# Optimization experiments

Measured on AMD Instinct MI355X. Metric: run time of the kernel, lower is better.

## Reference

```python
import jax, jax.numpy as jnp
import numpy as np

NUM_HEADS = 12
LN_EPS = 1e-5


def _layernorm(x, w, b):
    m = jnp.mean(x, axis=-1, keepdims=True)
    v = jnp.mean(jnp.square(x - m), axis=-1, keepdims=True)
    return (x - m) * jax.lax.rsqrt(v + LN_EPS) * w + b


def setup_inputs() -> dict:
    key = jax.random.key(0)
    ks = jax.random.split(key, 6)
    B, N, C, H = 8, 1024, 768, 3072
    s = 0.02
    return {
        "x": jax.random.normal(ks[0], (B, N, C), jnp.float32),
        "ln1_w": jnp.ones((C,), jnp.float32),
        "ln1_b": jnp.zeros((C,), jnp.float32),
        "qkv_w": jax.random.normal(ks[1], (3 * C, C), jnp.float32) * s,
        "qkv_b": jnp.zeros((3 * C,), jnp.float32),
        "proj_w": jax.random.normal(ks[2], (C, C), jnp.float32) * s,
        "proj_b": jnp.zeros((C,), jnp.float32),
        "ln2_w": jnp.ones((C,), jnp.float32),
        "ln2_b": jnp.zeros((C,), jnp.float32),
        "fc1_w": jax.random.normal(ks[3], (H, C), jnp.float32) * s,
        "fc1_b": jnp.zeros((H,), jnp.float32),
        "fc2_w": jax.random.normal(ks[4], (C, H), jnp.float32) * s,
        "fc2_b": jnp.zeros((C,), jnp.float32),
    }


def reference(x, ln1_w, ln1_b, qkv_w, qkv_b, proj_w, proj_b,
              ln2_w, ln2_b, fc1_w, fc1_b, fc2_w, fc2_b):
    B, N, C = x.shape
    H = NUM_HEADS
    d = C // H
    scale = d ** (-0.5)

    # --- attention on norm1(x) (size=None path, dropout rates are 0) ---
    h = _layernorm(x, ln1_w, ln1_b)
    qkv = h @ qkv_w.T + qkv_b                      # [B,N,3C]
    qkv = qkv.reshape(B, N, 3, H, d).transpose(2, 0, 3, 1, 4)  # [3,B,H,N,d]
    q, k, v = qkv[0], qkv[1], qkv[2]
    attn = jnp.einsum('bhqd,bhkd->bhqk', q, k) * scale
    attn = jax.nn.softmax(attn, axis=-1)
    o = jnp.einsum('bhqk,bhkd->bhqd', attn, v)     # [B,H,N,d]
    o = o.transpose(0, 2, 1, 3).reshape(B, N, C)
    x_attn = o @ proj_w.T + proj_b

    # --- residual + MLP ---
    x = x + x_attn
    h2 = _layernorm(x, ln2_w, ln2_b)
    h2 = jax.nn.gelu(h2 @ fc1_w.T + fc1_b, approximate=False)
    x = x + (h2 @ fc2_w.T + fc2_b)
    return x
```

## Files before the change

kernel.cpp:

```cpp
#include <hip/hip_runtime.h>
#include <cmath>

typedef __bf16 bf16;
typedef __bf16 bf16x8 __attribute__((ext_vector_type(8)));
typedef __bf16 bf16x4 __attribute__((ext_vector_type(4)));
typedef float floatx4 __attribute__((ext_vector_type(4)));

#define MFMA16(A, B, C) __builtin_amdgcn_mfma_f32_16x16x32_bf16((A), (B), (C), 0, 0, 0)

#define GLDS16(g, l)                                                   \
  __builtin_amdgcn_global_load_lds(                                    \
      (const __attribute__((address_space(1))) void*)(g),              \
      (__attribute__((address_space(3))) void*)(l), 16, 0, 0)

__global__ __launch_bounds__(256) void f2b4_kernel(
    const float* __restrict__ s0, bf16* __restrict__ d0, int n0,
    const float* __restrict__ s1, bf16* __restrict__ d1, int n1,
    const float* __restrict__ s2, bf16* __restrict__ d2, int n2,
    const float* __restrict__ s3, bf16* __restrict__ d3, int n3) {
  int i = blockIdx.x * 256 + threadIdx.x;
  const float* s;
  bf16* d;
  if (i < n0) { s = s0 + (size_t)i * 4; d = d0 + (size_t)i * 4; }
  else if ((i -= n0) < n1) { s = s1 + (size_t)i * 4; d = d1 + (size_t)i * 4; }
  else if ((i -= n1) < n2) { s = s2 + (size_t)i * 4; d = d2 + (size_t)i * 4; }
  else if ((i -= n2) < n3) { s = s3 + (size_t)i * 4; d = d3 + (size_t)i * 4; }
  else return;
  bf16x4 v;
  v[0] = (bf16)s[0]; v[1] = (bf16)s[1]; v[2] = (bf16)s[2]; v[3] = (bf16)s[3];
  *(bf16x4*)d = v;
}

__global__ __launch_bounds__(256) void ln_kernel(const float* __restrict__ x,
                                                 const float* __restrict__ g,
                                                 const float* __restrict__ be,
                                                 bf16* __restrict__ out) {
  int row = blockIdx.x;
  int t = threadIdx.x;
  const float* xr = x + (size_t)row * 768;
  float v0 = xr[t], v1 = xr[t + 256], v2 = xr[t + 512];
  float s = v0 + v1 + v2;
  float s2 = v0 * v0 + v1 * v1 + v2 * v2;
#pragma unroll
  for (int o = 1; o < 64; o <<= 1) {
    s += __shfl_xor(s, o, 64);
    s2 += __shfl_xor(s2, o, 64);
  }
  __shared__ float red[8];
  int w = t >> 6, lane = t & 63;
  if (lane == 0) { red[w] = s; red[4 + w] = s2; }
  __syncthreads();
  float ts = red[0] + red[1] + red[2] + red[3];
  float ts2 = red[4] + red[5] + red[6] + red[7];
  float mean = ts * (1.0f / 768.0f);
  float var = ts2 * (1.0f / 768.0f) - mean * mean;
  float rstd = rsqrtf(var + 1e-5f);
  bf16* orow = out + (size_t)row * 768;
  orow[t]       = (bf16)((v0 - mean) * rstd * g[t]       + be[t]);
  orow[t + 256] = (bf16)((v1 - mean) * rstd * g[t + 256] + be[t + 256]);
  orow[t + 512] = (bf16)((v2 - mean) * rstd * g[t + 512] + be[t + 512]);
}

__global__ __launch_bounds__(256) void reduce_ln_kernel(
    const bf16* __restrict__ pp, const float* __restrict__ bias,
    const float* __restrict__ x, const float* __restrict__ g,
    const float* __restrict__ be, float* __restrict__ x1,
    bf16* __restrict__ h2) {
  int row = blockIdx.x;
  int t = threadIdx.x;
  const bf16* p0 = pp + (size_t)row * 768;
  const bf16* p1 = pp + (size_t)(8192 + row) * 768;
  const float* xr = x + (size_t)row * 768;
  float v0 = (float)p0[t]       + (float)p1[t]       + bias[t]       + xr[t];
  float v1 = (float)p0[t + 256] + (float)p1[t + 256] + bias[t + 256] + xr[t + 256];
  float v2 = (float)p0[t + 512] + (float)p1[t + 512] + bias[t + 512] + xr[t + 512];
  float* x1r = x1 + (size_t)row * 768;
  x1r[t] = v0; x1r[t + 256] = v1; x1r[t + 512] = v2;
  float s = v0 + v1 + v2;
  float s2 = v0 * v0 + v1 * v1 + v2 * v2;
#pragma unroll
  for (int o = 1; o < 64; o <<= 1) {
    s += __shfl_xor(s, o, 64);
    s2 += __shfl_xor(s2, o, 64);
  }
  __shared__ float red[8];
  int w = t >> 6, lane = t & 63;
  if (lane == 0) { red[w] = s; red[4 + w] = s2; }
  __syncthreads();
  float ts = red[0] + red[1] + red[2] + red[3];
  float ts2 = red[4] + red[5] + red[6] + red[7];
  float mean = ts * (1.0f / 768.0f);
  float var = ts2 * (1.0f / 768.0f) - mean * mean;
  float rstd = rsqrtf(var + 1e-5f);
  bf16* orow = h2 + (size_t)row * 768;
  orow[t]       = (bf16)((v0 - mean) * rstd * g[t]       + be[t]);
  orow[t + 256] = (bf16)((v1 - mean) * rstd * g[t + 256] + be[t + 256]);
  orow[t + 512] = (bf16)((v2 - mean) * rstd * g[t + 512] + be[t + 512]);
}

__global__ __launch_bounds__(256) void reduce_out_kernel(
    const bf16* __restrict__ pp, const float* __restrict__ bias,
    const float* __restrict__ x1, float* __restrict__ out) {
  int i = blockIdx.x * 256 + threadIdx.x;
  size_t base = (size_t)i * 4;
  int col = (int)(base % 768);
  bf16x4 a = *(const bf16x4*)(pp + base);
  bf16x4 b = *(const bf16x4*)(pp + (size_t)8192 * 768 + base);
  float4 xr = *(const float4*)(x1 + base);
  float4 r;
  r.x = (float)a[0] + (float)b[0] + bias[col]     + xr.x;
  r.y = (float)a[1] + (float)b[1] + bias[col + 1] + xr.y;
  r.z = (float)a[2] + (float)b[2] + bias[col + 2] + xr.z;
  r.w = (float)a[3] + (float)b[3] + bias[col + 3] + xr.w;
  *(float4*)(out + base) = r;
}

constexpr int EP_BF16 = 0;
constexpr int EP_PART = 1;
constexpr int EP_GELU_BF16 = 2;

template <int EP>
__global__ __launch_bounds__(256, 3) void gemm_bt(
    const bf16* __restrict__ A, const bf16* __restrict__ Bw,
    const float* __restrict__ bias,
    void* __restrict__ outp, int M, int N, int K) {
  __shared__ alignas(16) bf16 Asl[128 * 32];
  __shared__ alignas(16) bf16 Bsl[128 * 32];
  int tid = threadIdx.x;
  int lane = tid & 63, w = tid >> 6;
  int wm = w >> 1, wn = w & 1;
  int q16 = lane & 15, quad = lane >> 4;
  int fid = blockIdx.x + gridDim.x * blockIdx.y;
  int nb = gridDim.x;
  int s = fid >> 3;
  int m0 = ((fid & 7) * (gridDim.y >> 3) + s / nb) * 128;
  int n0 = (s % nb) * 128;
  int kz = blockIdx.z;
  int Ksub = K / gridDim.z;
  int kbeg = kz * Ksub;

  floatx4 acc[4][4];
#pragma unroll
  for (int i = 0; i < 4; i++)
#pragma unroll
    for (int j = 0; j < 4; j++) acc[i][j] = (floatx4){0.f, 0.f, 0.f, 0.f};

  int rA = (lane >> 2), c8 = (lane & 3) * 8;
  const bf16* a0 = A + (size_t)(m0 + (w * 2 + 0) * 16 + rA) * K + kbeg + c8;
  const bf16* a1 = A + (size_t)(m0 + (w * 2 + 1) * 16 + rA) * K + kbeg + c8;
  const bf16* b0 = Bw + (size_t)(n0 + (w * 2 + 0) * 16 + rA) * K + kbeg + c8;
  const bf16* b1 = Bw + (size_t)(n0 + (w * 2 + 1) * 16 + rA) * K + kbeg + c8;
  bf16* la0 = &Asl[w * 1024];
  bf16* la1 = &Asl[w * 1024 + 512];
  bf16* lb0 = &Bsl[w * 1024];
  bf16* lb1 = &Bsl[w * 1024 + 512];

  for (int k0 = 0; k0 < Ksub; k0 += 32) {
    __syncthreads();
    GLDS16(a0, la0);
    GLDS16(a1, la1);
    GLDS16(b0, lb0);
    GLDS16(b1, lb1);
    a0 += 32; a1 += 32; b0 += 32; b1 += 32;
    __syncthreads();
    bf16x8 af[4], bfr[4];
#pragma unroll
    for (int i = 0; i < 4; i++)
      af[i] = *(const bf16x8*)&Asl[(wm * 64 + i * 16 + q16) * 32 + quad * 8];
#pragma unroll
    for (int j = 0; j < 4; j++)
      bfr[j] = *(const bf16x8*)&Bsl[(wn * 64 + j * 16 + q16) * 32 + quad * 8];
#pragma unroll
    for (int i = 0; i < 4; i++)
#pragma unroll
      for (int j = 0; j < 4; j++) acc[i][j] = MFMA16(af[i], bfr[j], acc[i][j]);
  }

  bf16* opart = (bf16*)outp + (size_t)kz * M * N;
#pragma unroll
  for (int i = 0; i < 4; i++) {
#pragma unroll
    for (int j = 0; j < 4; j++) {
#pragma unroll
      for (int r = 0; r < 4; r++) {
        int m = m0 + wm * 64 + i * 16 + quad * 4 + r;
        int n = n0 + wn * 64 + j * 16 + q16;
        size_t idx = (size_t)m * N + n;
        if constexpr (EP == EP_PART) {
          opart[idx] = (bf16)acc[i][j][r];
        } else {
          float v = acc[i][j][r] + bias[n];
          if constexpr (EP == EP_BF16) {
            ((bf16*)outp)[idx] = (bf16)v;
          } else {
            float gv = 0.5f * v * (1.0f + erff(v * 0.70710678118654752f));
            ((bf16*)outp)[idx] = (bf16)gv;
          }
        }
      }
    }
  }
}

__global__ __launch_bounds__(256, 3) void attn_kernel(const bf16* __restrict__ qkv,
                                                      bf16* __restrict__ o) {
  __shared__ alignas(16) bf16 Kl[32 * 64];
  __shared__ alignas(16) bf16 Vt[64 * 5 * 8];
  __shared__ alignas(16) bf16 Pl[4][2][16 * 40];
  int tid = threadIdx.x;
  int lane = tid & 63, w = tid >> 6;
  int q16 = lane & 15, quad = lane >> 4;
  int b = blockIdx.y / 12, h = blockIdx.y % 12;
  int qbase = blockIdx.x * 128 + w * 32;

  bf16x8 qf[2][2];
#pragma unroll
  for (int qt = 0; qt < 2; qt++)
#pragma unroll
    for (int c = 0; c < 2; c++)
      qf[qt][c] = *(const bf16x8*)(qkv +
          (size_t)(b * 1024 + qbase + qt * 16 + q16) * 2304 + h * 64 +
          c * 32 + quad * 8);

  int kkey = w * 8 + (lane >> 3);
  int kchunk = (lane & 7) ^ (lane >> 3);
  const bf16* kg = qkv + (size_t)(b * 1024 + kkey) * 2304 + 768 + h * 64 +
                   (kchunk & 7) * 8;
  bf16* kl_dst = &Kl[w * 512];

  int kr = tid >> 3;
  int kcb = (tid & 7) * 8;
  const bf16* vg = qkv + (size_t)(b * 1024 + kr) * 2304 + 1536 + h * 64 + kcb;
  int vt_idx[8];
#pragma unroll
  for (int e = 0; e < 8; e++)
    vt_idx[e] = ((((kcb + e) * 5) + w) ^ (tid & 7)) * 8 + (kr & 7);

  int koff[2][2];
#pragma unroll
  for (int nc = 0; nc < 2; nc++)
#pragma unroll
    for (int ck = 0; ck < 2; ck++) {
      int key = nc * 16 + q16;
      koff[nc][ck] = (key * 8 + ((ck * 4 + quad) ^ (key & 7))) * 8;
    }
  int voff[4];
#pragma unroll
  for (int dc = 0; dc < 4; dc++) {
    int d = dc * 16 + q16;
    voff[dc] = ((d * 5 + quad) ^ ((d >> 3) & 7)) * 8;
  }
  const bf16* pread = &Pl[w][0][q16 * 40 + quad * 8];
  int pw_base = (quad * 4) * 40 + q16;

  float l_[2][4];
  floatx4 oacc[2][4];
#pragma unroll
  for (int qt = 0; qt < 2; qt++)
#pragma unroll
    for (int r = 0; r < 4; r++) l_[qt][r] = 0.f;
#pragma unroll
  for (int qt = 0; qt < 2; qt++)
#pragma unroll
    for (int dc = 0; dc < 4; dc++) oacc[qt][dc] = (floatx4){0.f, 0.f, 0.f, 0.f};

  for (int kt = 0; kt < 32; kt++) {
    __syncthreads();
    GLDS16(kg, kl_dst);
    bf16x8 vv = *(const bf16x8*)vg;
    kg += 32 * 2304;
    vg += 32 * 2304;
#pragma unroll
    for (int e = 0; e < 8; e++) Vt[vt_idx[e]] = vv[e];
    __syncthreads();

    bf16x8 kf[2][2];
#pragma unroll
    for (int nc = 0; nc < 2; nc++)
#pragma unroll
      for (int ck = 0; ck < 2; ck++)
        kf[nc][ck] = *(const bf16x8*)&Kl[koff[nc][ck]];

#pragma unroll
    for (int qt = 0; qt < 2; qt++) {
#pragma unroll
      for (int nc = 0; nc < 2; nc++) {
        floatx4 z = (floatx4){0.f, 0.f, 0.f, 0.f};
        z = MFMA16(qf[qt][0], kf[nc][0], z);
        z = MFMA16(qf[qt][1], kf[nc][1], z);
#pragma unroll
        for (int r = 0; r < 4; r++) {
          float p = __builtin_amdgcn_exp2f(z[r] * 0.18033688011f);
          l_[qt][r] += p;
          Pl[w][qt][pw_base + r * 40 + nc * 16] = (bf16)p;
        }
      }
    }
    __syncthreads();

    bf16x8 vf[4];
#pragma unroll
    for (int dc = 0; dc < 4; dc++) vf[dc] = *(const bf16x8*)&Vt[voff[dc]];
#pragma unroll
    for (int qt = 0; qt < 2; qt++) {
      bf16x8 pf = *(const bf16x8*)(pread + qt * 640);
#pragma unroll
      for (int dc = 0; dc < 4; dc++)
        oacc[qt][dc] = MFMA16(pf, vf[dc], oacc[qt][dc]);
    }
  }

#pragma unroll
  for (int qt = 0; qt < 2; qt++) {
    bf16* op = o + (size_t)(b * 1024 + qbase + qt * 16) * 768 + h * 64;
#pragma unroll
    for (int r = 0; r < 4; r++) {
      float s = l_[qt][r];
#pragma unroll
      for (int off = 1; off < 16; off <<= 1) s += __shfl_xor(s, off, 16);
      float inv = 1.0f / s;
#pragma unroll
      for (int dc = 0; dc < 4; dc++)
        op[(size_t)(quad * 4 + r) * 768 + dc * 16 + q16] =
            (bf16)(oacc[qt][dc][r] * inv);
    }
  }
}

extern "C" void kernel_launch(void* const* d_in, const int* in_sizes, int n_in,
                              void* d_out, int out_size, void* d_ws, size_t ws_size,
                              hipStream_t stream) {
  (void)in_sizes; (void)n_in; (void)out_size; (void)ws_size;
  const float* x      = (const float*)d_in[0];
  const float* ln1_w  = (const float*)d_in[1];
  const float* ln1_b  = (const float*)d_in[2];
  const float* qkv_w  = (const float*)d_in[3];
  const float* qkv_b  = (const float*)d_in[4];
  const float* proj_w = (const float*)d_in[5];
  const float* proj_b = (const float*)d_in[6];
  const float* ln2_w  = (const float*)d_in[7];
  const float* ln2_b  = (const float*)d_in[8];
  const float* fc1_w  = (const float*)d_in[9];
  const float* fc1_b  = (const float*)d_in[10];
  const float* fc2_w  = (const float*)d_in[11];
  const float* fc2_b  = (const float*)d_in[12];

  char* ws = (char*)d_ws;
  size_t off = 0;
  auto alloc = [&](size_t bytes) {
    void* p = ws + off;
    off += (bytes + 255) & ~(size_t)255;
    return p;
  };
  bf16* wq  = (bf16*)alloc((size_t)2304 * 768 * 2);
  bf16* wp  = (bf16*)alloc((size_t)768 * 768 * 2);
  bf16* wf1 = (bf16*)alloc((size_t)3072 * 768 * 2);
  bf16* wf2 = (bf16*)alloc((size_t)768 * 3072 * 2);
  bf16* slotA = (bf16*)alloc((size_t)8192 * 768 * 2);
  bf16* slotB = (bf16*)alloc((size_t)8192 * 3072 * 2);
  float* x1 = (float*)alloc((size_t)8192 * 768 * 4);
  bf16* part = (bf16*)alloc((size_t)2 * 8192 * 768 * 2);

  bf16* h1 = slotA;
  bf16* qkvb = slotB;
  bf16* ob = slotA;
  bf16* h2 = slotA;
  bf16* hm = slotB;

  f2b4_kernel<<<6912, 256, 0, stream>>>(
      qkv_w, wq, 2304 * 768 / 4, proj_w, wp, 768 * 768 / 4,
      fc1_w, wf1, 3072 * 768 / 4, fc2_w, wf2, 768 * 3072 / 4);

  ln_kernel<<<8192, 256, 0, stream>>>(x, ln1_w, ln1_b, h1);
  gemm_bt<EP_BF16><<<dim3(18, 64, 1), 256, 0, stream>>>(h1, wq, qkv_b, qkvb,
                                                        8192, 2304, 768);
  attn_kernel<<<dim3(8, 96), 256, 0, stream>>>(qkvb, ob);
  gemm_bt<EP_PART><<<dim3(6, 64, 2), 256, 0, stream>>>(ob, wp, nullptr, part,
                                                       8192, 768, 768);
  reduce_ln_kernel<<<8192, 256, 0, stream>>>(part, proj_b, x, ln2_w, ln2_b,
                                             x1, h2);
  gemm_bt<EP_GELU_BF16><<<dim3(24, 64, 1), 256, 0, stream>>>(h2, wf1, fc1_b, hm,
                                                             8192, 3072, 768);
  gemm_bt<EP_PART><<<dim3(6, 64, 2), 256, 0, stream>>>(hm, wf2, nullptr, part,
                                                       8192, 768, 3072);
  reduce_out_kernel<<<6144, 256, 0, stream>>>(part, fc2_b, x1, (float*)d_out);
}
```

Baseline: 372.6 us.

## Deepen GEMM K-tile to 64 with XOR swizzle, fuse LN1 with weight cast, approximate GELU

```diff
diff --git a/kernel.cpp b/kernel.cpp
--- a/kernel.cpp
+++ b/kernel.cpp
@@ -13,12 +13,41 @@
       (const __attribute__((address_space(1))) void*)(g),              \
       (__attribute__((address_space(3))) void*)(l), 16, 0, 0)
 
-__global__ __launch_bounds__(256) void f2b4_kernel(
+__global__ __launch_bounds__(256) void pre_kernel(
+    const float* __restrict__ x, const float* __restrict__ g,
+    const float* __restrict__ be, bf16* __restrict__ h1,
     const float* __restrict__ s0, bf16* __restrict__ d0, int n0,
     const float* __restrict__ s1, bf16* __restrict__ d1, int n1,
     const float* __restrict__ s2, bf16* __restrict__ d2, int n2,
     const float* __restrict__ s3, bf16* __restrict__ d3, int n3) {
-  int i = blockIdx.x * 256 + threadIdx.x;
+  int bid = blockIdx.x;
+  int t = threadIdx.x;
+  if (bid < 8192) {
+    const float* xr = x + (size_t)bid * 768;
+    float v0 = xr[t], v1 = xr[t + 256], v2 = xr[t + 512];
+    float s = v0 + v1 + v2;
+    float s2 = v0 * v0 + v1 * v1 + v2 * v2;
+#pragma unroll
+    for (int o = 1; o < 64; o <<= 1) {
+      s += __shfl_xor(s, o, 64);
+      s2 += __shfl_xor(s2, o, 64);
+    }
+    __shared__ float red[8];
+    int w = t >> 6, lane = t & 63;
+    if (lane == 0) { red[w] = s; red[4 + w] = s2; }
+    __syncthreads();
+    float ts = red[0] + red[1] + red[2] + red[3];
+    float ts2 = red[4] + red[5] + red[6] + red[7];
+    float mean = ts * (1.0f / 768.0f);
+    float var = ts2 * (1.0f / 768.0f) - mean * mean;
+    float rstd = rsqrtf(var + 1e-5f);
+    bf16* orow = h1 + (size_t)bid * 768;
+    orow[t]       = (bf16)((v0 - mean) * rstd * g[t]       + be[t]);
+    orow[t + 256] = (bf16)((v1 - mean) * rstd * g[t + 256] + be[t + 256]);
+    orow[t + 512] = (bf16)((v2 - mean) * rstd * g[t + 512] + be[t + 512]);
+    return;
+  }
+  int i = (bid - 8192) * 256 + t;
   const float* s;
   bf16* d;
   if (i < n0) { s = s0 + (size_t)i * 4; d = d0 + (size_t)i * 4; }
@@ -29,36 +58,6 @@
   bf16x4 v;
   v[0] = (bf16)s[0]; v[1] = (bf16)s[1]; v[2] = (bf16)s[2]; v[3] = (bf16)s[3];
   *(bf16x4*)d = v;
-}
-
-__global__ __launch_bounds__(256) void ln_kernel(const float* __restrict__ x,
-                                                 const float* __restrict__ g,
-                                                 const float* __restrict__ be,
-                                                 bf16* __restrict__ out) {
-  int row = blockIdx.x;
-  int t = threadIdx.x;
-  const float* xr = x + (size_t)row * 768;
-  float v0 = xr[t], v1 = xr[t + 256], v2 = xr[t + 512];
-  float s = v0 + v1 + v2;
-  float s2 = v0 * v0 + v1 * v1 + v2 * v2;
-#pragma unroll
-  for (int o = 1; o < 64; o <<= 1) {
-    s += __shfl_xor(s, o, 64);
-    s2 += __shfl_xor(s2, o, 64);
-  }
-  __shared__ float red[8];
-  int w = t >> 6, lane = t & 63;
-  if (lane == 0) { red[w] = s; red[4 + w] = s2; }
-  __syncthreads();
-  float ts = red[0] + red[1] + red[2] + red[3];
-  float ts2 = red[4] + red[5] + red[6] + red[7];
-  float mean = ts * (1.0f / 768.0f);
-  float var = ts2 * (1.0f / 768.0f) - mean * mean;
-  float rstd = rsqrtf(var + 1e-5f);
-  bf16* orow = out + (size_t)row * 768;
-  orow[t]       = (bf16)((v0 - mean) * rstd * g[t]       + be[t]);
-  orow[t + 256] = (bf16)((v1 - mean) * rstd * g[t + 256] + be[t + 256]);
-  orow[t + 512] = (bf16)((v2 - mean) * rstd * g[t + 512] + be[t + 512]);
 }
 
 __global__ __launch_bounds__(256) void reduce_ln_kernel(
@@ -124,8 +123,8 @@
     const bf16* __restrict__ A, const bf16* __restrict__ Bw,
     const float* __restrict__ bias,
     void* __restrict__ outp, int M, int N, int K) {
-  __shared__ alignas(16) bf16 Asl[128 * 32];
-  __shared__ alignas(16) bf16 Bsl[128 * 32];
+  __shared__ alignas(16) bf16 Asl[128 * 64];
+  __shared__ alignas(16) bf16 Bsl[128 * 64];
   int tid = threadIdx.x;
   int lane = tid & 63, w = tid >> 6;
   int wm = w >> 1, wn = w & 1;
@@ -145,35 +144,52 @@
 #pragma unroll
     for (int j = 0; j < 4; j++) acc[i][j] = (floatx4){0.f, 0.f, 0.f, 0.f};
 
-  int rA = (lane >> 2), c8 = (lane & 3) * 8;
-  const bf16* a0 = A + (size_t)(m0 + (w * 2 + 0) * 16 + rA) * K + kbeg + c8;
-  const bf16* a1 = A + (size_t)(m0 + (w * 2 + 1) * 16 + rA) * K + kbeg + c8;
-  const bf16* b0 = Bw + (size_t)(n0 + (w * 2 + 0) * 16 + rA) * K + kbeg + c8;
-  const bf16* b1 = Bw + (size_t)(n0 + (w * 2 + 1) * 16 + rA) * K + kbeg + c8;
-  bf16* la0 = &Asl[w * 1024];
-  bf16* la1 = &Asl[w * 1024 + 512];
-  bf16* lb0 = &Bsl[w * 1024];
-  bf16* lb1 = &Bsl[w * 1024 + 512];
-
-  for (int k0 = 0; k0 < Ksub; k0 += 32) {
-    __syncthreads();
-    GLDS16(a0, la0);
-    GLDS16(a1, la1);
-    GLDS16(b0, lb0);
-    GLDS16(b1, lb1);
-    a0 += 32; a1 += 32; b0 += 32; b1 += 32;
-    __syncthreads();
-    bf16x8 af[4], bfr[4];
-#pragma unroll
-    for (int i = 0; i < 4; i++)
-      af[i] = *(const bf16x8*)&Asl[(wm * 64 + i * 16 + q16) * 32 + quad * 8];
-#pragma unroll
-    for (int j = 0; j < 4; j++)
-      bfr[j] = *(const bf16x8*)&Bsl[(wn * 64 + j * 16 + q16) * 32 + quad * 8];
-#pragma unroll
-    for (int i = 0; i < 4; i++)
-#pragma unroll
-      for (int j = 0; j < 4; j++) acc[i][j] = MFMA16(af[i], bfr[j], acc[i][j]);
+  int rIn = lane >> 3;
+  int cg = (lane & 7) ^ rIn;
+  const bf16* ag[4];
+  const bf16* bg[4];
+#pragma unroll
+  for (int q = 0; q < 4; q++) {
+    int ca = w * 4 + q;
+    ag[q] = A + (size_t)(m0 + ca * 8 + rIn) * K + kbeg + cg * 8;
+    bg[q] = Bw + (size_t)(n0 + ca * 8 + rIn) * K + kbeg + cg * 8;
+  }
+  bf16* la = &Asl[w * 2048];
+  bf16* lb = &Bsl[w * 2048];
+
+  int msel = q16 & 7;
+  int offA[2][4], offB[2][4];
+#pragma unroll
+  for (int ks = 0; ks < 2; ks++) {
+#pragma unroll
+    for (int i = 0; i < 4; i++) {
+      offA[ks][i] = (wm * 64 + i * 16 + q16) * 64 + (((ks * 4 + quad) ^ msel)) * 8;
+      offB[ks][i] = (wn * 64 + i * 16 + q16) * 64 + (((ks * 4 + quad) ^ msel)) * 8;
+    }
+  }
+
+  for (int k0 = 0; k0 < Ksub; k0 += 64) {
+    __syncthreads();
+#pragma unroll
+    for (int q = 0; q < 4; q++) {
+      GLDS16(ag[q], la + q * 512);
+      GLDS16(bg[q], lb + q * 512);
+      ag[q] += 64;
+      bg[q] += 64;
+    }
+    __syncthreads();
+#pragma unroll
+    for (int ks = 0; ks < 2; ks++) {
+      bf16x8 af[4], bfr[4];
+#pragma unroll
+      for (int i = 0; i < 4; i++) af[i] = *(const bf16x8*)&Asl[offA[ks][i]];
+#pragma unroll
+      for (int j = 0; j < 4; j++) bfr[j] = *(const bf16x8*)&Bsl[offB[ks][j]];
+#pragma unroll
+      for (int i = 0; i < 4; i++)
+#pragma unroll
+        for (int j = 0; j < 4; j++) acc[i][j] = MFMA16(af[i], bfr[j], acc[i][j]);
+    }
   }
 
   bf16* opart = (bf16*)outp + (size_t)kz * M * N;
@@ -193,7 +209,9 @@
           if constexpr (EP == EP_BF16) {
             ((bf16*)outp)[idx] = (bf16)v;
           } else {
-            float gv = 0.5f * v * (1.0f + erff(v * 0.70710678118654752f));
+            float u = v * (2.3022083f + 0.1029443f * v * v);
+            float e = __builtin_amdgcn_exp2f(-u);
+            float gv = v * __builtin_amdgcn_rcpf(1.0f + e);
             ((bf16*)outp)[idx] = (bf16)gv;
           }
         }
@@ -367,11 +385,11 @@
   bf16* h2 = slotA;
   bf16* hm = slotB;
 
-  f2b4_kernel<<<6912, 256, 0, stream>>>(
+  pre_kernel<<<8192 + 6912, 256, 0, stream>>>(
+      x, ln1_w, ln1_b, h1,
       qkv_w, wq, 2304 * 768 / 4, proj_w, wp, 768 * 768 / 4,
       fc1_w, wf1, 3072 * 768 / 4, fc2_w, wf2, 768 * 3072 / 4);
 
-  ln_kernel<<<8192, 256, 0, stream>>>(x, ln1_w, ln1_b, h1);
   gemm_bt<EP_BF16><<<dim3(18, 64, 1), 256, 0, stream>>>(h1, wq, qkv_b, qkvb,
                                                         8192, 2304, 768);
   attn_kernel<<<dim3(8, 96), 256, 0, stream>>>(qkvb, ob);
```

Result: faster. 334.2 us (-10.3%).
